# Optimization experiments

Measured on AMD Instinct MI355X. Metric: run time of the kernel, lower is better.

The kernel has to match this reference:

```python
import jax, jax.numpy as jnp
import numpy as np
import math

FACTOR = 5  # module default

def setup_inputs() -> dict:
    key = jax.random.key(0)
    kq, kk, kv, ki = jax.random.split(key, 4)
    B, L, S, H, D = 2, 4096, 4096, 8, 64
    u_part = min(FACTOR * math.ceil(math.log(L)), S)  # 45: sampled keys per query
    return {
        "queries": jax.random.normal(kq, (B, L, H, D), jnp.float32),
        "keys": jax.random.normal(kk, (B, S, H, D), jnp.float32),
        "values": jax.random.normal(kv, (B, S, H, D), jnp.float32),
        "index_sample": jax.random.randint(ki, (L, u_part), 0, S),
    }

def reference(queries, keys, values, index_sample):
    # queries: [B,L,H,D], keys/values: [B,S,H,D], index_sample: [L,u_part]
    B, L, H, D = queries.shape
    S = keys.shape[1]
    Q = jnp.transpose(queries, (0, 2, 1, 3))  # [B,H,L,D]
    K = jnp.transpose(keys, (0, 2, 1, 3))     # [B,H,S,D]
    V = jnp.transpose(values, (0, 2, 1, 3))   # [B,H,S,D]
    U_part = min(FACTOR * math.ceil(math.log(S)), L)  # n_top queries (static)

    # --- _prob_QK: sample keys, sparsity measure M, top-k queries ---
    K_sample = K[:, :, index_sample, :]  # gather -> [B,H,L,u_part,D]
    QK_sample = jnp.einsum('bhld,bhlud->bhlu', Q, K_sample)  # [B,H,L,u_part]
    M = QK_sample.max(axis=-1) - QK_sample.sum(axis=-1) / S  # [B,H,L]
    _, M_top = jax.lax.top_k(M, U_part)                      # [B,H,U_part]
    Q_reduce = jnp.take_along_axis(Q, M_top[..., None], axis=2)  # [B,H,U_part,D]
    scores = jnp.einsum('bhud,bhsd->bhus', Q_reduce, K)          # [B,H,U_part,S]

    # --- mask_flag=False branch: plain scaled softmax attention ---
    scale = 1.0 / math.sqrt(D)
    attn = jax.nn.softmax(scores * scale, axis=-1)  # [B,H,U_part,S]
    context = jnp.einsum('bhus,bhsd->bhud', attn, V)  # [B,H,U_part,D]
    return context, attn
```

## Files before the change

### kernel.cpp

```cpp
#include <hip/hip_runtime.h>

#define BB 2
#define LL 4096
#define SS 4096
#define HH 8
#define DD 64
#define UU 45
#define SCALE 0.125f
#define NCH 32
#define CHK 128

__global__ __launch_bounds__(256) void k_compute_M(
    const float* __restrict__ q, const float* __restrict__ k,
    const int* __restrict__ idx, float* __restrict__ M) {
  __shared__ int sidx[16 * UU];
  int tid = threadIdx.x;
  int bh = blockIdx.x & 15;
  int l0 = (blockIdx.x >> 4) << 4;
  for (int i = tid; i < 16 * UU; i += 256) sidx[i] = idx[(long)l0 * UU + i];
  __syncthreads();

  int slot = tid >> 4;
  int sub  = tid & 15;
  int l = l0 + slot;
  int b = bh >> 3, h = bh & 7;

  const float4* qp = (const float4*)(q + (((long)b * LL + l) * HH + h) * DD);
  float4 qq = qp[sub];
  const float* kb = k + (long)b * SS * HH * DD + h * DD;

  float mx = -INFINITY, sm = 0.f;
  #pragma unroll 9
  for (int u = 0; u < UU; ++u) {
    int s = sidx[slot * UU + u];
    float4 kk4 = ((const float4*)(kb + (long)s * (HH * DD)))[sub];
    float p = qq.x * kk4.x + qq.y * kk4.y + qq.z * kk4.z + qq.w * kk4.w;
    #pragma unroll
    for (int off = 8; off; off >>= 1) p += __shfl_xor(p, off, 16);
    mx = fmaxf(mx, p);
    sm += p;
  }
  if (sub == 0) M[(long)bh * LL + l] = mx - sm * (1.0f / SS);
}

__global__ __launch_bounds__(256) void k_topk(
    const float* __restrict__ M, int* __restrict__ Mtop) {
  __shared__ unsigned keys[LL];
  __shared__ int hist[256];
  __shared__ int wsum[4];
  __shared__ int sh_bin, sh_gtwin;
  __shared__ int ccount, ecount;
  __shared__ unsigned cand_key[64];
  __shared__ int cand_idx[64];
  __shared__ int elist[LL];

  int bh = blockIdx.x, tid = threadIdx.x;
  int lane = tid & 63, w = tid >> 6;
  const float* m = M + (long)bh * LL;
  for (int i = tid; i < LL; i += 256) {
    union { float f; unsigned u; } cv; cv.f = m[i];
    keys[i] = (cv.u & 0x80000000u) ? ~cv.u : (cv.u | 0x80000000u);
  }
  if (tid == 0) { ccount = 0; ecount = 0; }
  __syncthreads();

  unsigned prefix = 0, pmask = 0;
  int need = UU, above = 0;

  for (int shift = 24; shift >= 0; shift -= 8) {
    hist[tid] = 0;
    __syncthreads();
    #pragma unroll
    for (int j = 0; j < 16; ++j) {
      unsigned kk = keys[tid + (j << 8)];
      if ((kk & pmask) == prefix) atomicAdd(&hist[(kk >> shift) & 255], 1);
    }
    __syncthreads();
    int v = hist[tid];
    int sfx = v;
    #pragma unroll
    for (int st = 1; st < 64; st <<= 1) {
      int o = __shfl_down(sfx, st, 64);
      if (lane + st < 64) sfx += o;
    }
    if (lane == 0) wsum[w] = sfx;
    __syncthreads();
    for (int t = w + 1; t < 4; ++t) sfx += wsum[t];
    int gt = sfx - v;
    if (gt < need && sfx >= need) {
      sh_bin = tid;
      sh_gtwin = gt;
    }
    __syncthreads();
    prefix |= ((unsigned)sh_bin << shift);
    pmask  |= (255u << shift);
    need  -= sh_gtwin;
    above += sh_gtwin;
    __syncthreads();
  }
  unsigned T = prefix;

  #pragma unroll
  for (int j = 0; j < 16; ++j) {
    int i = tid + (j << 8);
    unsigned kk = keys[i];
    if (kk > T)      { int p = atomicAdd(&ccount, 1); cand_key[p] = kk; cand_idx[p] = i; }
    else if (kk == T){ int p = atomicAdd(&ecount, 1); elist[p] = i; }
  }
  __syncthreads();
  int nc = ccount, ne = ecount;
  for (int t = tid; t < nc; t += 256) {
    unsigned kk = cand_key[t]; int ii = cand_idx[t]; int r = 0;
    for (int j = 0; j < nc; ++j)
      r += (cand_key[j] > kk) || (cand_key[j] == kk && cand_idx[j] < ii);
    Mtop[bh * UU + r] = ii;
  }
  for (int t = tid; t < ne; t += 256) {
    int ii = elist[t]; int r = 0;
    for (int j = 0; j < ne; ++j) r += (elist[j] < ii);
    if (r < need) Mtop[bh * UU + above + r] = ii;
  }
}

__global__ __launch_bounds__(256) void k_fused(
    const float* __restrict__ q, const float* __restrict__ k,
    const float* __restrict__ v, const int* __restrict__ Mtop,
    float* __restrict__ attn, float* __restrict__ part,
    float* __restrict__ stats) {
  __shared__ float smem[4 * UU * DD];
  __shared__ float gl[UU];
  float* qr = smem;
  float* sp = smem + UU * DD;

  int ch = blockIdx.x, bh = blockIdx.y;
  int b = bh >> 3, h = bh & 7;
  int tid = threadIdx.x;
  int lane = tid & 63, w = tid >> 6;
  int s0 = ch * CHK;

  for (int i = tid; i < UU * DD; i += 256) {
    int u = i >> 6, d = i & 63;
    int l = Mtop[bh * UU + u];
    qr[i] = q[(((long)b * LL + l) * HH + h) * DD + d];
  }
  __syncthreads();

  {
    int slb = tid & 63;
    int uq  = tid >> 6;
    const float4* kp0 = (const float4*)(k + (((long)b * SS + s0 + slb) * HH + h) * DD);
    const float4* kp1 = (const float4*)(k + (((long)b * SS + s0 + slb + 64) * HH + h) * DD);
    float4 kr0[16], kr1[16];
    #pragma unroll
    for (int j = 0; j < 16; ++j) { kr0[j] = kp0[j]; kr1[j] = kp1[j]; }
    int ub = (uq == 0) ? 0 : 12 + (uq - 1) * 11;
    int ue = ub + ((uq == 0) ? 12 : 11);
    for (int u = ub; u < ue; ++u) {
      const float4* qp = (const float4*)(qr + u * DD);
      float a0 = 0.f, a1 = 0.f, c0 = 0.f, c1 = 0.f;
      #pragma unroll
      for (int j = 0; j < 8; ++j) {
        float4 qA = qp[j], qB = qp[j + 8];
        float4 kA0 = kr0[j], kB0 = kr0[j + 8];
        float4 kA1 = kr1[j], kB1 = kr1[j + 8];
        a0 += qA.x * kA0.x + qA.y * kA0.y + qA.z * kA0.z + qA.w * kA0.w;
        a1 += qB.x * kB0.x + qB.y * kB0.y + qB.z * kB0.z + qB.w * kB0.w;
        c0 += qA.x * kA1.x + qA.y * kA1.y + qA.z * kA1.z + qA.w * kA1.w;
        c1 += qB.x * kB1.x + qB.y * kB1.y + qB.z * kB1.z + qB.w * kB1.w;
      }
      sp[slb * 52 + u]        = __expf((a0 + a1) * SCALE);
      sp[(slb + 64) * 52 + u] = __expf((c0 + c1) * SCALE);
    }
  }
  __syncthreads();

  for (int i = tid; i < UU * CHK; i += 256) {
    int u = i >> 7, sl = i & 127;
    attn[((long)bh * UU + u) * SS + s0 + sl] = sp[sl * 52 + u];
  }
  for (int u = w; u < UU; u += 4) {
    float e = sp[lane * 52 + u] + sp[(lane + 64) * 52 + u];
    #pragma unroll
    for (int off = 32; off; off >>= 1) e += __shfl_xor(e, off, 64);
    if (lane == 0) gl[u] = e;
  }
  float acc[UU];
  #pragma unroll
  for (int u = 0; u < UU; ++u) acc[u] = 0.f;
  const float* vb = v + (long)b * SS * HH * DD + h * DD + lane;
  #pragma unroll 2
  for (int j = 0; j < 32; ++j) {
    int sl = (j << 2) + w;
    float vd = vb[(long)(s0 + sl) * (HH * DD)];
    const float* ar = sp + sl * 52;
    #pragma unroll
    for (int g = 0; g < 11; ++g) {
      float4 aa = *(const float4*)(ar + g * 4);
      acc[g * 4 + 0] += aa.x * vd;
      acc[g * 4 + 1] += aa.y * vd;
      acc[g * 4 + 2] += aa.z * vd;
      acc[g * 4 + 3] += aa.w * vd;
    }
    acc[44] += ar[44] * vd;
  }

  __syncthreads();
  #pragma unroll
  for (int u = 0; u < UU; ++u) smem[(w * UU + u) * DD + lane] = acc[u];
  __syncthreads();
  long base = ((long)bh * NCH + ch) * (UU * DD);
  for (int i = tid; i < UU * DD; i += 256)
    part[base + i] = smem[i] + smem[UU * DD + i] + smem[2 * UU * DD + i] + smem[3 * UU * DD + i];
  if (tid < UU)
    stats[((long)bh * UU + tid) * NCH + ch] = gl[tid];
}

__global__ __launch_bounds__(256) void k_epilogue(
    const float* __restrict__ stats, const float* __restrict__ part,
    float* __restrict__ attn, float* __restrict__ ctx) {
  __shared__ float sinv;
  int bid = blockIdx.x, tid = threadIdx.x;
  if (bid < BB * HH * UU) {
    long row = bid;
    const float* st = stats + row * NCH;
    if (tid == 0) {
      float L = 0.f;
      #pragma unroll
      for (int c = 0; c < NCH; ++c) L += st[c];
      sinv = 1.0f / L;
    }
    __syncthreads();
    float inv = sinv;
    float4* a = (float4*)(attn + row * SS);
    #pragma unroll
    for (int g = 0; g < 4; ++g) {
      int i4 = g * 256 + tid;
      float4 vv = a[i4];
      vv.x *= inv; vv.y *= inv; vv.z *= inv; vv.w *= inv;
      a[i4] = vv;
    }
  } else {
    int e = (bid - BB * HH * UU) * 256 + tid;
    int bh = e / (UU * DD);
    int r = e - bh * (UU * DD);
    int u = r >> 6;
    const float* st = stats + ((long)bh * UU + u) * NCH;
    float L = 0.f, s = 0.f;
    #pragma unroll
    for (int c = 0; c < NCH; ++c) {
      L += st[c];
      s += part[((long)bh * NCH + c) * (UU * DD) + r];
    }
    ctx[e] = s / L;
  }
}

__global__ __launch_bounds__(256) void k_scores(
    const float* __restrict__ q, const float* __restrict__ k,
    const int* __restrict__ Mtop, float* __restrict__ attn) {
  __shared__ float qr[UU * DD];
  int bh = blockIdx.y;
  int b = bh >> 3, h = bh & 7;
  for (int i = threadIdx.x; i < UU * DD; i += 256) {
    int u = i >> 6, d = i & 63;
    int l = Mtop[bh * UU + u];
    qr[i] = q[(((long)b * LL + l) * HH + h) * DD + d];
  }
  __syncthreads();
  int s = blockIdx.x * 256 + threadIdx.x;
  float4 kr[16];
  const float4* kp = (const float4*)(k + (((long)b * SS + s) * HH + h) * DD);
  #pragma unroll
  for (int j = 0; j < 16; ++j) kr[j] = kp[j];
  for (int u = 0; u < UU; ++u) {
    const float4* qp = (const float4*)(qr + u * DD);
    float acc = 0.f;
    #pragma unroll
    for (int j = 0; j < 16; ++j) {
      float4 qq = qp[j];
      acc += qq.x * kr[j].x + qq.y * kr[j].y + qq.z * kr[j].z + qq.w * kr[j].w;
    }
    attn[((long)bh * UU + u) * SS + s] = acc * SCALE;
  }
}

__global__ __launch_bounds__(256) void k_softmax(float* __restrict__ attn) {
  __shared__ float red[256];
  long row = blockIdx.x;
  float* a = attn + row * SS;
  float v[16];
  float mx = -INFINITY;
  #pragma unroll
  for (int j = 0; j < 16; ++j) {
    v[j] = a[j * 256 + threadIdx.x];
    mx = fmaxf(mx, v[j]);
  }
  red[threadIdx.x] = mx;
  __syncthreads();
  for (int st = 128; st; st >>= 1) {
    if (threadIdx.x < st) red[threadIdx.x] = fmaxf(red[threadIdx.x], red[threadIdx.x + st]);
    __syncthreads();
  }
  mx = red[0];
  __syncthreads();
  float sm = 0.f;
  #pragma unroll
  for (int j = 0; j < 16; ++j) {
    v[j] = __expf(v[j] - mx);
    sm += v[j];
  }
  red[threadIdx.x] = sm;
  __syncthreads();
  for (int st = 128; st; st >>= 1) {
    if (threadIdx.x < st) red[threadIdx.x] += red[threadIdx.x + st];
    __syncthreads();
  }
  float inv = 1.0f / red[0];
  #pragma unroll
  for (int j = 0; j < 16; ++j) a[j * 256 + threadIdx.x] = v[j] * inv;
}

__global__ __launch_bounds__(256) void k_context_fb(
    const float* __restrict__ attn, const float* __restrict__ v,
    float* __restrict__ ctx) {
  __shared__ float red[4][DD];
  int row = blockIdx.x;
  int bh = row / UU;
  int b = bh >> 3, h = bh & 7;
  int lane = threadIdx.x & 63;
  int grp = threadIdx.x >> 6;
  const float* a = attn + (long)row * SS;
  float acc = 0.f;
  for (int s = grp; s < SS; s += 4)
    acc += a[s] * v[(((long)b * SS + s) * HH + h) * DD + lane];
  red[grp][lane] = acc;
  __syncthreads();
  if (grp == 0)
    ctx[(long)row * DD + lane] = red[0][lane] + red[1][lane] + red[2][lane] + red[3][lane];
}

extern "C" void kernel_launch(void* const* d_in, const int* in_sizes, int n_in,
                              void* d_out, int out_size, void* d_ws, size_t ws_size,
                              hipStream_t stream) {
  const float* q   = (const float*)d_in[0];
  const float* k   = (const float*)d_in[1];
  const float* v   = (const float*)d_in[2];
  const int*   idx = (const int*)d_in[3];

  float* out  = (float*)d_out;
  float* ctx  = out;
  float* attn = out + (long)BB * HH * UU * DD;

  float* M    = attn;
  int*   Mtop = (int*)ctx;

  k_compute_M<<<BB * HH * LL / 16, 256, 0, stream>>>(q, k, idx, M);
  k_topk<<<BB * HH, 256, 0, stream>>>(M, Mtop);

  size_t part_bytes  = (size_t)BB * HH * NCH * UU * DD * sizeof(float);
  size_t stats_bytes = (size_t)BB * HH * UU * NCH * sizeof(float);
  if (ws_size >= part_bytes + stats_bytes) {
    float* part  = (float*)d_ws;
    float* stats = (float*)((char*)d_ws + part_bytes);
    k_fused<<<dim3(NCH, BB * HH), 256, 0, stream>>>(q, k, v, Mtop, attn, part, stats);
    int nctx = (BB * HH * UU * DD) / 256;
    k_epilogue<<<BB * HH * UU + nctx, 256, 0, stream>>>(stats, part, attn, ctx);
  } else {
    k_scores<<<dim3(SS / 256, BB * HH), 256, 0, stream>>>(q, k, Mtop, attn);
    k_softmax<<<BB * HH * UU, 256, 0, stream>>>(attn);
    k_context_fb<<<BB * HH * UU, 256, 0, stream>>>(attn, v, ctx);
  }
}
```

Before: 104.5 us.

## Bucket sampled indices and compute sparsity measure via LDS-tiled key sweep

```diff
diff --git a/kernel.cpp b/kernel.cpp
--- a/kernel.cpp
+++ b/kernel.cpp
@@ -9,6 +9,133 @@
 #define SCALE 0.125f
 #define NCH 32
 #define CHK 128
+#define GCH 256
+#define GTS 64
+
+__global__ __launch_bounds__(256) void k_hist(
+    const int* __restrict__ idx, int* __restrict__ hist) {
+  int e = blockIdx.x * 256 + threadIdx.x;
+  int l = e / UU;
+  int s = idx[e];
+  atomicAdd(&hist[(l >> 8) * 64 + (s >> 6)], 1);
+}
+
+__global__ __launch_bounds__(256) void k_scan(
+    const int* __restrict__ hist, int* __restrict__ off) {
+  __shared__ int tmp[256];
+  int tid = threadIdx.x;
+  int v0 = hist[tid*4], v1 = hist[tid*4+1], v2 = hist[tid*4+2], v3 = hist[tid*4+3];
+  int ts = v0 + v1 + v2 + v3;
+  tmp[tid] = ts;
+  __syncthreads();
+  for (int st = 1; st < 256; st <<= 1) {
+    int add = (tid >= st) ? tmp[tid - st] : 0;
+    __syncthreads();
+    tmp[tid] += add;
+    __syncthreads();
+  }
+  int run = tmp[tid] - ts;
+  off[tid*4] = run; run += v0;
+  off[tid*4+1] = run; run += v1;
+  off[tid*4+2] = run; run += v2;
+  off[tid*4+3] = run; run += v3;
+  if (tid == 255) off[1024] = run;
+}
+
+__global__ __launch_bounds__(256) void k_scatter(
+    const int* __restrict__ idx, const int* __restrict__ off,
+    int* __restrict__ cursor, unsigned* __restrict__ entries) {
+  int e = blockIdx.x * 256 + threadIdx.x;
+  int l = e / UU, u = e - l * UU;
+  int s = idx[e];
+  int bkt = (l >> 8) * 64 + (s >> 6);
+  int pos = atomicAdd(&cursor[bkt], 1);
+  entries[off[bkt] + pos] =
+      ((unsigned)s << 14) | ((unsigned)(l & 255) << 6) | (unsigned)u;
+}
+
+__device__ __forceinline__ void proc_entry(
+    unsigned ent, const float* Qt, const float* Kt, float* dots, int sub) {
+  int sl = (ent >> 14) & 63;
+  int ll = (ent >> 6) & 255;
+  int uu = ent & 63;
+  float4 kk = ((const float4*)Kt)[sl * 16 + sub];
+  float4 qv = ((const float4*)Qt)[ll * 16 + sub];
+  float p = qv.x * kk.x + qv.y * kk.y + qv.z * kk.z + qv.w * kk.w;
+  p += __shfl_xor(p, 8, 16);
+  p += __shfl_xor(p, 4, 16);
+  p += __shfl_xor(p, 2, 16);
+  p += __shfl_xor(p, 1, 16);
+  if (sub == 0) dots[ll * UU + uu] = p;
+}
+
+__global__ __launch_bounds__(256, 1) void k_gather_M(
+    const float* __restrict__ q, const float* __restrict__ k,
+    const unsigned* __restrict__ entries, const int* __restrict__ off,
+    float* __restrict__ M) {
+  __shared__ float Qt[GCH * DD];
+  __shared__ float dots[GCH * UU];
+  __shared__ float Kt[GTS * DD];
+  int tid = threadIdx.x;
+  int bh = blockIdx.x & 15;
+  int chunk = blockIdx.x >> 4;
+  int b = bh >> 3, h = bh & 7;
+  int l0 = chunk * GCH;
+  int g = tid >> 4, sub = tid & 15;
+
+  const float4* qb4 = (const float4*)q;
+  for (int i4 = tid; i4 < GCH * 16; i4 += 256)
+    ((float4*)Qt)[i4] = qb4[(((long)b * LL + l0 + (i4 >> 4)) * HH + h) * 16 + (i4 & 15)];
+
+  const float4* kb4 = (const float4*)(k + ((long)b * SS * HH + h) * DD);
+  #pragma unroll
+  for (int j = 0; j < 4; ++j) {
+    int fi = j * 256 + tid;
+    ((float4*)Kt)[fi] = kb4[(long)(fi >> 4) * 128 + (fi & 15)];
+  }
+  __syncthreads();
+
+  for (int t = 0; t < 64; ++t) {
+    float4 s0, s1, s2, s3;
+    if (t < 63) {
+      int base = (t + 1) * GTS;
+      int f0 = tid, f1 = 256 + tid, f2 = 512 + tid, f3 = 768 + tid;
+      s0 = kb4[(long)(base + (f0 >> 4)) * 128 + (f0 & 15)];
+      s1 = kb4[(long)(base + (f1 >> 4)) * 128 + (f1 & 15)];
+      s2 = kb4[(long)(base + (f2 >> 4)) * 128 + (f2 & 15)];
+      s3 = kb4[(long)(base + (f3 >> 4)) * 128 + (f3 & 15)];
+    }
+    int eb = off[(chunk << 6) + t];
+    int ee = off[(chunk << 6) + t + 1];
+    int e = eb + g;
+    for (; e + 48 < ee; e += 64) {
+      unsigned n0 = entries[e], n1 = entries[e + 16];
+      unsigned n2 = entries[e + 32], n3 = entries[e + 48];
+      proc_entry(n0, Qt, Kt, dots, sub);
+      proc_entry(n1, Qt, Kt, dots, sub);
+      proc_entry(n2, Qt, Kt, dots, sub);
+      proc_entry(n3, Qt, Kt, dots, sub);
+    }
+    for (; e < ee; e += 16) proc_entry(entries[e], Qt, Kt, dots, sub);
+    __syncthreads();
+    if (t < 63) {
+      ((float4*)Kt)[tid] = s0;
+      ((float4*)Kt)[256 + tid] = s1;
+      ((float4*)Kt)[512 + tid] = s2;
+      ((float4*)Kt)[768 + tid] = s3;
+    }
+    __syncthreads();
+  }
+
+  float mx = -INFINITY, sm = 0.f;
+  #pragma unroll
+  for (int u = 0; u < UU; ++u) {
+    float p = dots[tid * UU + u];
+    mx = fmaxf(mx, p);
+    sm += p;
+  }
+  M[(long)bh * LL + l0 + tid] = mx - sm * (1.0f / SS);
+}
 
 __global__ __launch_bounds__(256) void k_compute_M(
     const float* __restrict__ q, const float* __restrict__ k,
@@ -19,18 +146,14 @@
   int l0 = (blockIdx.x >> 4) << 4;
   for (int i = tid; i < 16 * UU; i += 256) sidx[i] = idx[(long)l0 * UU + i];
   __syncthreads();
-
-  int slot = tid >> 4;
-  int sub  = tid & 15;
+  int slot = tid >> 4, sub = tid & 15;
   int l = l0 + slot;
   int b = bh >> 3, h = bh & 7;
-
   const float4* qp = (const float4*)(q + (((long)b * LL + l) * HH + h) * DD);
   float4 qq = qp[sub];
   const float* kb = k + (long)b * SS * HH * DD + h * DD;
-
   float mx = -INFINITY, sm = 0.f;
-  #pragma unroll 9
+  #pragma unroll 5
   for (int u = 0; u < UU; ++u) {
     int s = sidx[slot * UU + u];
     float4 kk4 = ((const float4*)(kb + (long)s * (HH * DD)))[sub];
@@ -194,12 +317,12 @@
     float vd = vb[(long)(s0 + sl) * (HH * DD)];
     const float* ar = sp + sl * 52;
     #pragma unroll
-    for (int g = 0; g < 11; ++g) {
-      float4 aa = *(const float4*)(ar + g * 4);
-      acc[g * 4 + 0] += aa.x * vd;
-      acc[g * 4 + 1] += aa.y * vd;
-      acc[g * 4 + 2] += aa.z * vd;
-      acc[g * 4 + 3] += aa.w * vd;
+    for (int g2 = 0; g2 < 11; ++g2) {
+      float4 aa = *(const float4*)(ar + g2 * 4);
+      acc[g2 * 4 + 0] += aa.x * vd;
+      acc[g2 * 4 + 1] += aa.y * vd;
+      acc[g2 * 4 + 2] += aa.z * vd;
+      acc[g2 * 4 + 3] += aa.w * vd;
     }
     acc[44] += ar[44] * vd;
   }
@@ -354,14 +477,31 @@
   float* M    = attn;
   int*   Mtop = (int*)ctx;
 
-  k_compute_M<<<BB * HH * LL / 16, 256, 0, stream>>>(q, k, idx, M);
-  k_topk<<<BB * HH, 256, 0, stream>>>(M, Mtop);
-
   size_t part_bytes  = (size_t)BB * HH * NCH * UU * DD * sizeof(float);
   size_t stats_bytes = (size_t)BB * HH * UU * NCH * sizeof(float);
+  size_t bkt_bytes   = (1024 + 1024 + 1025) * sizeof(int);
+  size_t need_new    = part_bytes + stats_bytes + bkt_bytes;
+
+  char* pw = (char*)d_ws;
+  float* part  = (float*)pw;
+  float* stats = (float*)(pw + part_bytes);
+  int*   hist  = (int*)(pw + part_bytes + stats_bytes);
+  int*   cursor = hist + 1024;
+  int*   off    = hist + 2048;
+  unsigned* entries = (unsigned*)pw;
+
+  if (ws_size >= need_new) {
+    hipMemsetAsync(hist, 0, 2048 * sizeof(int), stream);
+    k_hist<<<720, 256, 0, stream>>>(idx, hist);
+    k_scan<<<1, 256, 0, stream>>>(hist, off);
+    k_scatter<<<720, 256, 0, stream>>>(idx, off, cursor, entries);
+    k_gather_M<<<16 * 16, 256, 0, stream>>>(q, k, entries, off, M);
+  } else {
+    k_compute_M<<<BB * HH * LL / 16, 256, 0, stream>>>(q, k, idx, M);
+  }
+  k_topk<<<BB * HH, 256, 0, stream>>>(M, Mtop);
+
   if (ws_size >= part_bytes + stats_bytes) {
-    float* part  = (float*)d_ws;
-    float* stats = (float*)((char*)d_ws + part_bytes);
     k_fused<<<dim3(NCH, BB * HH), 256, 0, stream>>>(q, k, v, Mtop, attn, part, stats);
     int nctx = (BB * HH * UU * DD) / 256;
     k_epilogue<<<BB * HH * UU + nctx, 256, 0, stream>>>(stats, part, attn, ctx);
```

New measurement: 348.6 us. 3.34x slower.
